# Optimization experiments

Measured on AMD Instinct MI355X. Metric: run time of the kernel, lower is better.

## Reference

```python
import jax, jax.numpy as jnp
import numpy as np

B, S, H, D = 2, 2048, 16, 64
DIM = H * D          # 1024, fused QKV dense outputs 3*DIM
EPS = 1e-6
NINF = -10000.0      # additive mask value from module
STD = 0.02           # truncated-normal init stddev (plain normal here)


def setup_inputs() -> dict:
    key = jax.random.key(0)
    k0, k1, k2 = jax.random.split(key, 3)
    x = jax.random.normal(k0, (B, S, DIM), jnp.float32)
    ln_g = jnp.ones((DIM,), jnp.float32)
    ln_b = jnp.zeros((DIM,), jnp.float32)
    wqkv = jax.random.normal(k1, (DIM, 3 * DIM), jnp.float32) * STD
    bqkv = jnp.zeros((3 * DIM,), jnp.float32)
    wo = jax.random.normal(k2, (DIM, DIM), jnp.float32) * STD
    bo = jnp.zeros((DIM,), jnp.float32)
    return {"x": x, "ln_g": ln_g, "ln_b": ln_b, "wqkv": wqkv,
            "bqkv": bqkv, "wo": wo, "bo": bo}


def reference(x, ln_g, ln_b, wqkv, bqkv, wo, bo):
    b, s, _ = x.shape
    # pre-norm LayerNorm (axis=-1, eps=1e-6)
    mu = jnp.mean(x, axis=-1, keepdims=True)
    var = jnp.mean(jnp.square(x - mu), axis=-1, keepdims=True)
    h = (x - mu) * jax.lax.rsqrt(var + EPS) * ln_g + ln_b
    # fused QKV projection, split along feature axis
    qkv = h @ wqkv + bqkv                       # [b, s, 3*DIM]
    q, k, v = jnp.split(qkv, 3, axis=2)

    def heads(t):                               # [b, s, DIM] -> [b, H, s, D]
        return t.reshape(b, s, H, D).transpose(0, 2, 1, 3)

    q, k, v = heads(q), heads(k), heads(v)
    scores = jnp.einsum("bhqd,bhkd->bhqk", q, k) / jnp.sqrt(jnp.float32(D))
    # causal mask: positions j > i get ninf (mask=None path, Lq == Lk)
    causal = (jnp.arange(s)[:, None] < jnp.arange(s)[None, :]).astype(jnp.float32) * NINF
    a = jax.nn.softmax(scores + causal, axis=-1)  # attdrop rate 0 -> identity
    ctx = jnp.einsum("bhqk,bhkd->bhqd", a, v)
    ctx = ctx.transpose(0, 2, 1, 3).reshape(b, s, DIM)
    # output dense + residual (drop rate 0 -> identity)
    return x + ctx @ wo + bo
```

## Files before the change

kernel.cpp:

```cpp
#include <hip/hip_runtime.h>
#include <hip/hip_bf16.h>

#define B_   2
#define S_   2048
#define H_   16
#define D_   64
#define DIM_ 1024
#define QKV_SZ (32 * 2048 * 64)

typedef __attribute__((ext_vector_type(8))) short bf16x8;
typedef __attribute__((ext_vector_type(4))) float f32x4;
typedef unsigned short u16;
typedef unsigned int u32;

static __device__ __forceinline__ u16 f2bf(float f) {
    union { float f; unsigned u; } v; v.f = f;
    unsigned u = v.u;
    unsigned r = (u + 0x7fffu + ((u >> 16) & 1u)) >> 16;
    return (u16)r;
}
static __device__ __forceinline__ float exp2_fast(float x) {
    float r; asm("v_exp_f32 %0, %1" : "=v"(r) : "v"(x)); return r;
}
static __device__ __forceinline__ u32 cvtpk_bf16(float lo, float hi) {
    u32 r; asm("v_cvt_pk_bf16_f32 %0, %1, %2" : "=v"(r) : "v"(lo), "v"(hi)); return r;
}
static __device__ __forceinline__ void gload_lds16(const u16* g, u16* l) {
    __builtin_amdgcn_global_load_lds(
        (const __attribute__((address_space(1))) void*)g,
        (__attribute__((address_space(3))) void*)l, 16, 0, 0);
}

__global__ __launch_bounds__(256) void prep_kernel(
    const float* __restrict__ x, const float* __restrict__ g,
    const float* __restrict__ b, u16* __restrict__ hb,
    const float* __restrict__ wqkv, u16* __restrict__ wqkvT,
    const float* __restrict__ wo, u16* __restrict__ woT)
{
    __shared__ u16 T[64][65];
    __shared__ float rs[4], rss[4];
    int bid = blockIdx.x;
    int t = threadIdx.x;
    if (bid < 4096) {
        int row = bid;
        const float4 v = ((const float4*)(x + row * DIM_))[t];
        float s  = v.x + v.y + v.z + v.w;
        float ss = v.x*v.x + v.y*v.y + v.z*v.z + v.w*v.w;
#pragma unroll
        for (int m = 1; m < 64; m <<= 1) { s += __shfl_xor(s, m); ss += __shfl_xor(ss, m); }
        int wid = t >> 6, lane = t & 63;
        if (lane == 0) { rs[wid] = s; rss[wid] = ss; }
        __syncthreads();
        s  = rs[0] + rs[1] + rs[2] + rs[3];
        ss = rss[0] + rss[1] + rss[2] + rss[3];
        float mu   = s * (1.0f / DIM_);
        float var  = ss * (1.0f / DIM_) - mu * mu;
        float rstd = rsqrtf(var + 1e-6f);
        const float4 gv = ((const float4*)g)[t];
        const float4 bv = ((const float4*)b)[t];
        ushort4 ov;
        ov.x = f2bf((v.x - mu) * rstd * gv.x + bv.x);
        ov.y = f2bf((v.y - mu) * rstd * gv.y + bv.y);
        ov.z = f2bf((v.z - mu) * rstd * gv.z + bv.z);
        ov.w = f2bf((v.w - mu) * rstd * gv.w + bv.w);
        ((ushort4*)(hb + row * DIM_))[t] = ov;
    } else {
        const float* src; u16* dst; int R, C, c0, r0;
        if (bid < 4864) {
            int idx = bid - 4096;
            src = wqkv; dst = wqkvT; R = 1024; C = 3072;
            c0 = (idx % 48) * 64; r0 = (idx / 48) * 64;
        } else {
            int idx = bid - 4864;
            src = wo; dst = woT; R = 1024; C = 1024;
            c0 = (idx % 16) * 64; r0 = (idx / 16) * 64;
        }
        int rl = t >> 4, cl = (t & 15) * 4;
#pragma unroll
        for (int p = 0; p < 4; p++) {
            float4 v = *(const float4*)(src + (size_t)(r0 + rl + p * 16) * C + c0 + cl);
            T[cl + 0][rl + p * 16] = f2bf(v.x);
            T[cl + 1][rl + p * 16] = f2bf(v.y);
            T[cl + 2][rl + p * 16] = f2bf(v.z);
            T[cl + 3][rl + p * 16] = f2bf(v.w);
        }
        __syncthreads();
#pragma unroll
        for (int p = 0; p < 4; p++) {
            ushort4 o;
            o.x = T[rl + p * 16][cl + 0];
            o.y = T[rl + p * 16][cl + 1];
            o.z = T[rl + p * 16][cl + 2];
            o.w = T[rl + p * 16][cl + 3];
            *(ushort4*)(dst + (size_t)(c0 + rl + p * 16) * R + r0 + cl) = o;
        }
    }
}

__global__ __launch_bounds__(256) void qkv_gemm128(
    const u16* __restrict__ A, const u16* __restrict__ Bw,
    const float* __restrict__ bias, u16* __restrict__ qkv)
{
    __shared__ __align__(16) u16 As[2][128 * 32];
    __shared__ __align__(16) u16 Bs[2][128 * 32];
    int t = threadIdx.x;
    int bn = blockIdx.x * 128, bm = blockIdx.y * 128;
    int wid = t >> 6, lane = t & 63;
    int wm = wid >> 1, wn = wid & 1;
    int l15 = lane & 15, l4 = lane >> 4;

    f32x4 zero = {0.f, 0.f, 0.f, 0.f};
    f32x4 acc[4][4];
#pragma unroll
    for (int i = 0; i < 4; i++)
#pragma unroll
        for (int j = 0; j < 4; j++) acc[i][j] = zero;

    int scol = ((lane & 3) ^ ((lane >> 3) & 3)) * 8;
    const u16* aSrc = A  + (size_t)(bm + wid * 32 + (lane >> 2)) * 1024 + scol;
    const u16* bSrc = Bw + (size_t)(bn + wid * 32 + (lane >> 2)) * 1024 + scol;
    int rdk = ((l15 >> 1) & 3) << 4;

#define STAGE_G(bufsel, kk) do { \
        char* Ad = (char*)As + (bufsel) * 8192 + wid * 2048; \
        char* Bd = (char*)Bs + (bufsel) * 8192 + wid * 2048; \
        gload_lds16(aSrc + (kk),             (u16*)Ad); \
        gload_lds16(aSrc + (kk) + 16 * 1024, (u16*)(Ad + 1024)); \
        gload_lds16(bSrc + (kk),             (u16*)Bd); \
        gload_lds16(bSrc + (kk) + 16 * 1024, (u16*)(Bd + 1024)); \
    } while (0)

    STAGE_G(0, 0);
    __syncthreads();
    int cur = 0;
    for (int kt = 0; kt < 32; ++kt) {
        if (kt < 31) STAGE_G(cur ^ 1, (kt + 1) * 32);
        const char* Ab = (const char*)As + cur * 8192;
        const char* Bb = (const char*)Bs + cur * 8192;
        bf16x8 af[4], bf[4];
#pragma unroll
        for (int mi = 0; mi < 4; mi++)
            af[mi] = *(const bf16x8*)(Ab + (wm * 64 + mi * 16 + l15) * 64 + (l4 * 16 ^ rdk));
#pragma unroll
        for (int ni = 0; ni < 4; ni++)
            bf[ni] = *(const bf16x8*)(Bb + (wn * 64 + ni * 16 + l15) * 64 + (l4 * 16 ^ rdk));
        __builtin_amdgcn_s_setprio(1);
#pragma unroll
        for (int mi = 0; mi < 4; mi++)
#pragma unroll
            for (int ni = 0; ni < 4; ni++)
                acc[mi][ni] = __builtin_amdgcn_mfma_f32_16x16x32_bf16(af[mi], bf[ni], acc[mi][ni], 0, 0, 0);
        __builtin_amdgcn_s_setprio(0);
        __syncthreads();
        cur ^= 1;
    }
#pragma unroll
    for (int mi = 0; mi < 4; mi++)
#pragma unroll
        for (int ni = 0; ni < 4; ni++) {
            int col = bn + wn * 64 + ni * 16 + l15;
            int which = col >> 10, f = col & 1023;
            int hh = f >> 6, d = f & 63;
            float bs = bias[col];
            if (which == 2) {
                int s_base = bm + wm * 64 + mi * 16 + l4 * 4;
                int bb = s_base >> 11, s = s_base & 2047;
                ushort4 pk;
                pk.x = f2bf(acc[mi][ni][0] + bs);
                pk.y = f2bf(acc[mi][ni][1] + bs);
                pk.z = f2bf(acc[mi][ni][2] + bs);
                pk.w = f2bf(acc[mi][ni][3] + bs);
                *(ushort4*)(qkv + (size_t)2 * QKV_SZ +
                            ((size_t)(bb * 16 + hh) * 64 + d) * 2048 + s) = pk;
            } else {
                float scl = (which == 0) ? 0.18033688011112042f : 1.0f;
#pragma unroll
                for (int r = 0; r < 4; r++) {
                    int row = bm + wm * 64 + mi * 16 + l4 * 4 + r;
                    int bb = row >> 11, s = row & 2047;
                    qkv[(size_t)which * QKV_SZ + ((size_t)(bb * 16 + hh) * 2048 + s) * 64 + d] =
                        f2bf((acc[mi][ni][r] + bs) * scl);
                }
            }
        }
}

__global__ __launch_bounds__(256) void out_gemm128(
    const u16* __restrict__ A, const u16* __restrict__ Bw,
    const float* __restrict__ bias, const float* __restrict__ xres,
    float* __restrict__ out)
{
    __shared__ __align__(16) u16 As[2][128 * 32];
    __shared__ __align__(16) u16 Bs[2][64 * 32];
    int t = threadIdx.x;
    int bn = blockIdx.x * 64, bm = blockIdx.y * 128;
    int wid = t >> 6, lane = t & 63;
    int l15 = lane & 15, l4 = lane >> 4;

    f32x4 zero = {0.f, 0.f, 0.f, 0.f};
    f32x4 acc[2][4];
#pragma unroll
    for (int i = 0; i < 2; i++)
#pragma unroll
        for (int j = 0; j < 4; j++) acc[i][j] = zero;

    int scol = ((t & 3) ^ ((t >> 3) & 3)) * 8;
    const u16* aSrc = A  + (size_t)(bm + (t >> 2)) * 1024 + scol;
    const u16* bSrc = Bw + (size_t)(bn + (t >> 2)) * 1024 + scol;
    int rdk = ((l15 >> 1) & 3) << 4;

#define OSTG(bufsel, kk) do { \
        char* Ad = (char*)As + (bufsel) * 8192 + wid * 1024; \
        char* Bd = (char*)Bs + (bufsel) * 4096 + wid * 1024; \
        gload_lds16(aSrc + (kk),             (u16*)Ad); \
        gload_lds16(aSrc + (kk) + 64 * 1024, (u16*)(Ad + 4096)); \
        gload_lds16(bSrc + (kk),             (u16*)Bd); \
    } while (0)

    OSTG(0, 0);
    __syncthreads();
    int cur = 0;
    for (int kt = 0; kt < 32; ++kt) {
        if (kt < 31) OSTG(cur ^ 1, (kt + 1) * 32);
        const char* Ab = (const char*)As + cur * 8192;
        const char* Bb = (const char*)Bs + cur * 4096;
        bf16x8 af[2], bf[4];
#pragma unroll
        for (int mi = 0; mi < 2; mi++)
            af[mi] = *(const bf16x8*)(Ab + (wid * 32 + mi * 16 + l15) * 64 + (l4 * 16 ^ rdk));
#pragma unroll
        for (int ni = 0; ni < 4; ni++)
            bf[ni] = *(const bf16x8*)(Bb + (ni * 16 + l15) * 64 + (l4 * 16 ^ rdk));
        __builtin_amdgcn_s_setprio(1);
#pragma unroll
        for (int mi = 0; mi < 2; mi++)
#pragma unroll
            for (int ni = 0; ni < 4; ni++)
                acc[mi][ni] = __builtin_amdgcn_mfma_f32_16x16x32_bf16(af[mi], bf[ni], acc[mi][ni], 0, 0, 0);
        __builtin_amdgcn_s_setprio(0);
        __syncthreads();
        cur ^= 1;
    }
#pragma unroll
    for (int mi = 0; mi < 2; mi++)
#pragma unroll
        for (int ni = 0; ni < 4; ni++) {
            int col = bn + ni * 16 + l15;
            float bs = bias[col];
#pragma unroll
            for (int r = 0; r < 4; r++) {
                int row = bm + wid * 32 + mi * 16 + l4 * 4 + r;
                out[(size_t)row * 1024 + col] = xres[(size_t)row * 1024 + col] + acc[mi][ni][r] + bs;
            }
        }
}

__global__ __launch_bounds__(256) void attn_kernel(
    const u16* __restrict__ qbuf, const u16* __restrict__ kbuf,
    const u16* __restrict__ vbuf, u16* __restrict__ ctx)
{
    __shared__ __align__(16) char Ks[64 * 128];
    __shared__ __align__(16) char Vt[64 * 128];
    __shared__ __align__(16) char Pb[4 * 16 * 128];

    int t = threadIdx.x, wid = t >> 6, lane = t & 63;
    int l15 = lane & 15, l4 = lane >> 4;
    int idx = blockIdx.x;
    int qt = 31 - (idx >> 5);
    int bh = idx & 31;
    int q0 = qt * 64;
    int sr = t >> 3, g = t & 7;
    int bb = bh >> 4, hh = bh & 15;
    f32x4 zero = {0.f, 0.f, 0.f, 0.f};

    const u16* Q = qbuf + (size_t)(bh * 2048 + q0 + wid * 16) * 64;
    bf16x8 aq0 = *(const bf16x8*)(Q + l15 * 64 + 8 * l4);
    bf16x8 aq1 = *(const bf16x8*)(Q + l15 * 64 + 32 + 8 * l4);

    f32x4 o[4];
#pragma unroll
    for (int f = 0; f < 4; f++) o[f] = zero;
    float m_run = -1e30f;
    float l_run = 0.f;

    int kswz = (16 * g) ^ ((sr & 7) << 4);
    char* Pw = Pb + wid * 2048;
    int prow = l15 * 128;
    int pkey = (l15 & 7) << 4;
    int qloc = wid * 16 + l15;

    const u16* Kbase = kbuf + (size_t)bh * 2048 * 64;
    const u16* Vbase = vbuf + (size_t)bh * 64 * 2048;

    bf16x8 ck0 = *(const bf16x8*)(Kbase + (size_t)sr * 64 + g * 8);
    bf16x8 ck1 = *(const bf16x8*)(Kbase + (size_t)(sr + 32) * 64 + g * 8);
    bf16x8 cv0 = *(const bf16x8*)(Vbase + (size_t)sr * 2048 + g * 8);
    bf16x8 cv1 = *(const bf16x8*)(Vbase + (size_t)(sr + 32) * 2048 + g * 8);

    for (int kt = 0; kt <= qt; ++kt) {
        int nkt = (kt < qt) ? kt + 1 : qt;
        const u16* Kn = Kbase + (size_t)nkt * 64 * 64;
        const u16* Vn = Vbase + (size_t)nkt * 64;
        bf16x8 a = *(const bf16x8*)(Kn + (size_t)sr * 64 + g * 8);
        bf16x8 b = *(const bf16x8*)(Kn + (size_t)(sr + 32) * 64 + g * 8);
        bf16x8 c = *(const bf16x8*)(Vn + (size_t)sr * 2048 + g * 8);
        bf16x8 d = *(const bf16x8*)(Vn + (size_t)(sr + 32) * 2048 + g * 8);
        *(bf16x8*)(Ks + sr * 128 + kswz) = ck0;
        *(bf16x8*)(Ks + (sr + 32) * 128 + kswz) = ck1;
        *(bf16x8*)(Vt + sr * 128 + kswz) = cv0;
        *(bf16x8*)(Vt + (sr + 32) * 128 + kswz) = cv1;
        asm volatile("s_waitcnt lgkmcnt(0)" ::: "memory");
        __builtin_amdgcn_s_barrier();
        asm volatile("" ::: "memory");

        f32x4 sc[4];
        __builtin_amdgcn_s_setprio(1);
#pragma unroll
        for (int nf = 0; nf < 4; ++nf) {
            int krow = nf * 16 + l15;
            int kkey = (krow & 7) << 4;
            bf16x8 kb0 = *(const bf16x8*)(Ks + krow * 128 + ((16 * l4) ^ kkey));
            bf16x8 kb1 = *(const bf16x8*)(Ks + krow * 128 + ((64 + 16 * l4) ^ kkey));
            f32x4 z = zero;
            z = __builtin_amdgcn_mfma_f32_16x16x32_bf16(kb0, aq0, z, 0, 0, 0);
            z = __builtin_amdgcn_mfma_f32_16x16x32_bf16(kb1, aq1, z, 0, 0, 0);
            sc[nf] = z;
        }
        __builtin_amdgcn_s_setprio(0);

        if (kt == qt) {
#pragma unroll
            for (int nf = 0; nf < 4; nf++)
#pragma unroll
                for (int r = 0; r < 4; r++) {
                    int ka = nf * 16 + 4 * l4 + r;
                    if (ka > qloc) sc[nf][r] = -1e30f;
                }
        }
        float lmax = sc[0][0];
#pragma unroll
        for (int nf = 0; nf < 4; nf++)
#pragma unroll
            for (int r = 0; r < 4; r++) lmax = fmaxf(lmax, sc[nf][r]);
        if (__any(lmax > m_run + 10.f)) {
            float m0 = lmax;
            m0 = fmaxf(m0, __shfl_xor(m0, 16));
            m0 = fmaxf(m0, __shfl_xor(m0, 32));
            float mn = fmaxf(m_run, m0);
            float al = exp2_fast(m_run - mn);
            l_run *= al;
            m_run = mn;
            float a0 = __shfl(al, 4 * l4 + 0);
            float a1 = __shfl(al, 4 * l4 + 1);
            float a2 = __shfl(al, 4 * l4 + 2);
            float a3 = __shfl(al, 4 * l4 + 3);
#pragma unroll
            for (int f = 0; f < 4; f++) {
                o[f][0] *= a0; o[f][1] *= a1; o[f][2] *= a2; o[f][3] *= a3;
            }
        }
        float psum = 0.f;
#pragma unroll
        for (int nf = 0; nf < 4; nf++)
#pragma unroll
            for (int r = 0; r < 4; r++) {
                float pv = exp2_fast(sc[nf][r] - m_run);
                sc[nf][r] = pv; psum += pv;
            }
        l_run += psum;
#pragma unroll
        for (int nf = 0; nf < 4; nf++) {
            uint2 w;
            w.x = cvtpk_bf16(sc[nf][0], sc[nf][1]);
            w.y = cvtpk_bf16(sc[nf][2], sc[nf][3]);
            *(uint2*)(Pw + prow + ((nf * 32 + l4 * 8) ^ pkey)) = w;
        }
        __builtin_amdgcn_s_setprio(1);
#pragma unroll
        for (int kk = 0; kk < 2; kk++) {
            bf16x8 pa = *(const bf16x8*)(Pw + prow + ((64 * kk + 16 * l4) ^ pkey));
#pragma unroll
            for (int f = 0; f < 4; f++) {
                int vrow = f * 16 + l15;
                int vkey = (vrow & 7) << 4;
                bf16x8 vb = *(const bf16x8*)(Vt + vrow * 128 + ((64 * kk + 16 * l4) ^ vkey));
                o[f] = __builtin_amdgcn_mfma_f32_16x16x32_bf16(pa, vb, o[f], 0, 0, 0);
            }
        }
        __builtin_amdgcn_s_setprio(0);
        __syncthreads();
        ck0 = a; ck1 = b; cv0 = c; cv1 = d;
    }
    l_run += __shfl_xor(l_run, 16);
    l_run += __shfl_xor(l_run, 32);
#pragma unroll
    for (int r = 0; r < 4; r++) {
        float lr = __shfl(l_run, 4 * l4 + r);
        float inv = 1.f / lr;
        int qa = q0 + wid * 16 + l4 * 4 + r;
        u16* dst = ctx + (size_t)(bb * 2048 + qa) * 1024 + hh * 64;
#pragma unroll
        for (int f = 0; f < 4; f++) dst[f * 16 + l15] = f2bf(o[f][r] * inv);
    }
}

extern "C" void kernel_launch(void* const* d_in, const int* in_sizes, int n_in,
                              void* d_out, int out_size, void* d_ws, size_t ws_size,
                              hipStream_t stream)
{
    const float* x    = (const float*)d_in[0];
    const float* ln_g = (const float*)d_in[1];
    const float* ln_b = (const float*)d_in[2];
    const float* wqkv = (const float*)d_in[3];
    const float* bqkv = (const float*)d_in[4];
    const float* wo   = (const float*)d_in[5];
    const float* bo   = (const float*)d_in[6];
    float* out = (float*)d_out;

    char* ws = (char*)d_ws;
    u16* hbuf  = (u16*)ws;
    u16* qkvb  = (u16*)(ws + 8388608);
    u16* ctxb  = (u16*)(ws + 33554432);
    u16* wqkvT = ctxb;
    u16* woT   = (u16*)(ws + 41943040);

    prep_kernel<<<5120, 256, 0, stream>>>(x, ln_g, ln_b, hbuf, wqkv, wqkvT, wo, woT);
    qkv_gemm128<<<dim3(24, 32), 256, 0, stream>>>(hbuf, wqkvT, bqkv, qkvb);
    attn_kernel<<<1024, 256, 0, stream>>>(
        qkvb, qkvb + QKV_SZ, qkvb + 2 * QKV_SZ, ctxb);
    out_gemm128<<<dim3(16, 32), 256, 0, stream>>>(ctxb, woT, bo, x, out);
}
```

Measured before the change: 115.6 us.

## Enlarge attention query tile to 128 rows, two 16-row blocks per wave

Each attention block now handles 128 query rows instead of 64, and each wave processes two 16-row query sub-blocks. This reuses each K/V tile loaded into shared memory across twice as many queries, halving global K/V traffic and barrier count per query. The causal mask is generalized to per-element checks over the last tiles, and the block order is changed so the first 256 blocks take the longest tiles in descending order while the rest ascend. The grid halves to 512 blocks, which lowers parallelism and raises register pressure from the doubled accumulators.

```diff
diff --git a/kernel.cpp b/kernel.cpp
--- a/kernel.cpp
+++ b/kernel.cpp
@@ -261,33 +261,39 @@
 {
     __shared__ __align__(16) char Ks[64 * 128];
     __shared__ __align__(16) char Vt[64 * 128];
-    __shared__ __align__(16) char Pb[4 * 16 * 128];
+    __shared__ __align__(16) char Pb[4 * 32 * 128];
 
     int t = threadIdx.x, wid = t >> 6, lane = t & 63;
     int l15 = lane & 15, l4 = lane >> 4;
     int idx = blockIdx.x;
-    int qt = 31 - (idx >> 5);
-    int bh = idx & 31;
-    int q0 = qt * 64;
+    int qt, bh;
+    if (idx < 256) { qt = 15 - (idx >> 5); bh = idx & 31; }
+    else           { qt = (idx - 256) >> 5; bh = idx & 31; }
+    int q0 = qt * 128;
+    int ktE = 2 * qt + 1;
     int sr = t >> 3, g = t & 7;
     int bb = bh >> 4, hh = bh & 15;
     f32x4 zero = {0.f, 0.f, 0.f, 0.f};
 
-    const u16* Q = qbuf + (size_t)(bh * 2048 + q0 + wid * 16) * 64;
-    bf16x8 aq0 = *(const bf16x8*)(Q + l15 * 64 + 8 * l4);
-    bf16x8 aq1 = *(const bf16x8*)(Q + l15 * 64 + 32 + 8 * l4);
-
-    f32x4 o[4];
-#pragma unroll
-    for (int f = 0; f < 4; f++) o[f] = zero;
-    float m_run = -1e30f;
-    float l_run = 0.f;
+    const u16* Q = qbuf + (size_t)(bh * 2048 + q0 + wid * 32) * 64;
+    bf16x8 aq[2][2];
+#pragma unroll
+    for (int qb = 0; qb < 2; qb++)
+#pragma unroll
+        for (int h = 0; h < 2; h++)
+            aq[qb][h] = *(const bf16x8*)(Q + (qb * 16 + l15) * 64 + h * 32 + 8 * l4);
+
+    f32x4 o[2][4];
+#pragma unroll
+    for (int qb = 0; qb < 2; qb++)
+#pragma unroll
+        for (int f = 0; f < 4; f++) o[qb][f] = zero;
+    float m_run[2] = {-1e30f, -1e30f};
+    float l_run[2] = {0.f, 0.f};
 
     int kswz = (16 * g) ^ ((sr & 7) << 4);
-    char* Pw = Pb + wid * 2048;
-    int prow = l15 * 128;
+    char* Pw = Pb + wid * 4096;
     int pkey = (l15 & 7) << 4;
-    int qloc = wid * 16 + l15;
 
     const u16* Kbase = kbuf + (size_t)bh * 2048 * 64;
     const u16* Vbase = vbuf + (size_t)bh * 64 * 2048;
@@ -297,8 +303,8 @@
     bf16x8 cv0 = *(const bf16x8*)(Vbase + (size_t)sr * 2048 + g * 8);
     bf16x8 cv1 = *(const bf16x8*)(Vbase + (size_t)(sr + 32) * 2048 + g * 8);
 
-    for (int kt = 0; kt <= qt; ++kt) {
-        int nkt = (kt < qt) ? kt + 1 : qt;
+    for (int kt = 0; kt <= ktE; ++kt) {
+        int nkt = (kt < ktE) ? kt + 1 : ktE;
         const u16* Kn = Kbase + (size_t)nkt * 64 * 64;
         const u16* Vn = Vbase + (size_t)nkt * 64;
         bf16x8 a = *(const bf16x8*)(Kn + (size_t)sr * 64 + g * 8);
@@ -313,7 +319,7 @@
         __builtin_amdgcn_s_barrier();
         asm volatile("" ::: "memory");
 
-        f32x4 sc[4];
+        f32x4 sc[2][4];
         __builtin_amdgcn_s_setprio(1);
 #pragma unroll
         for (int nf = 0; nf < 4; ++nf) {
@@ -321,86 +327,115 @@
             int kkey = (krow & 7) << 4;
             bf16x8 kb0 = *(const bf16x8*)(Ks + krow * 128 + ((16 * l4) ^ kkey));
             bf16x8 kb1 = *(const bf16x8*)(Ks + krow * 128 + ((64 + 16 * l4) ^ kkey));
-            f32x4 z = zero;
-            z = __builtin_amdgcn_mfma_f32_16x16x32_bf16(kb0, aq0, z, 0, 0, 0);
-            z = __builtin_amdgcn_mfma_f32_16x16x32_bf16(kb1, aq1, z, 0, 0, 0);
-            sc[nf] = z;
+#pragma unroll
+            for (int qb = 0; qb < 2; qb++) {
+                f32x4 z = zero;
+                z = __builtin_amdgcn_mfma_f32_16x16x32_bf16(kb0, aq[qb][0], z, 0, 0, 0);
+                z = __builtin_amdgcn_mfma_f32_16x16x32_bf16(kb1, aq[qb][1], z, 0, 0, 0);
+                sc[qb][nf] = z;
+            }
         }
         __builtin_amdgcn_s_setprio(0);
 
-        if (kt == qt) {
+        if (kt * 64 + 63 > q0 + wid * 32) {
+#pragma unroll
+            for (int qb = 0; qb < 2; qb++)
+#pragma unroll
+                for (int nf = 0; nf < 4; nf++)
+#pragma unroll
+                    for (int r = 0; r < 4; r++) {
+                        int ka = kt * 64 + nf * 16 + 4 * l4 + r;
+                        int qg = q0 + wid * 32 + qb * 16 + l15;
+                        if (ka > qg) sc[qb][nf][r] = -1e30f;
+                    }
+        }
+        float lmax[2];
+#pragma unroll
+        for (int qb = 0; qb < 2; qb++) {
+            float lm = sc[qb][0][0];
 #pragma unroll
             for (int nf = 0; nf < 4; nf++)
 #pragma unroll
+                for (int r = 0; r < 4; r++) lm = fmaxf(lm, sc[qb][nf][r]);
+            lmax[qb] = lm;
+        }
+        bool need = (lmax[0] > m_run[0] + 10.f) | (lmax[1] > m_run[1] + 10.f);
+        if (__any(need)) {
+#pragma unroll
+            for (int qb = 0; qb < 2; qb++) {
+                float m0 = lmax[qb];
+                m0 = fmaxf(m0, __shfl_xor(m0, 16));
+                m0 = fmaxf(m0, __shfl_xor(m0, 32));
+                float mn = fmaxf(m_run[qb], m0);
+                float al = exp2_fast(m_run[qb] - mn);
+                l_run[qb] *= al;
+                m_run[qb] = mn;
+                float a0 = __shfl(al, 4 * l4 + 0);
+                float a1 = __shfl(al, 4 * l4 + 1);
+                float a2 = __shfl(al, 4 * l4 + 2);
+                float a3 = __shfl(al, 4 * l4 + 3);
+#pragma unroll
+                for (int f = 0; f < 4; f++) {
+                    o[qb][f][0] *= a0; o[qb][f][1] *= a1;
+                    o[qb][f][2] *= a2; o[qb][f][3] *= a3;
+                }
+            }
+        }
+#pragma unroll
+        for (int qb = 0; qb < 2; qb++) {
+            float psum = 0.f;
+#pragma unroll
+            for (int nf = 0; nf < 4; nf++)
+#pragma unroll
                 for (int r = 0; r < 4; r++) {
-                    int ka = nf * 16 + 4 * l4 + r;
-                    if (ka > qloc) sc[nf][r] = -1e30f;
+                    float pv = exp2_fast(sc[qb][nf][r] - m_run[qb]);
+                    sc[qb][nf][r] = pv; psum += pv;
                 }
-        }
-        float lmax = sc[0][0];
-#pragma unroll
-        for (int nf = 0; nf < 4; nf++)
-#pragma unroll
-            for (int r = 0; r < 4; r++) lmax = fmaxf(lmax, sc[nf][r]);
-        if (__any(lmax > m_run + 10.f)) {
-            float m0 = lmax;
-            m0 = fmaxf(m0, __shfl_xor(m0, 16));
-            m0 = fmaxf(m0, __shfl_xor(m0, 32));
-            float mn = fmaxf(m_run, m0);
-            float al = exp2_fast(m_run - mn);
-            l_run *= al;
-            m_run = mn;
-            float a0 = __shfl(al, 4 * l4 + 0);
-            float a1 = __shfl(al, 4 * l4 + 1);
-            float a2 = __shfl(al, 4 * l4 + 2);
-            float a3 = __shfl(al, 4 * l4 + 3);
-#pragma unroll
-            for (int f = 0; f < 4; f++) {
-                o[f][0] *= a0; o[f][1] *= a1; o[f][2] *= a2; o[f][3] *= a3;
-            }
-        }
-        float psum = 0.f;
-#pragma unroll
-        for (int nf = 0; nf < 4; nf++)
-#pragma unroll
-            for (int r = 0; r < 4; r++) {
-                float pv = exp2_fast(sc[nf][r] - m_run);
-                sc[nf][r] = pv; psum += pv;
-            }
-        l_run += psum;
-#pragma unroll
-        for (int nf = 0; nf < 4; nf++) {
-            uint2 w;
-            w.x = cvtpk_bf16(sc[nf][0], sc[nf][1]);
-            w.y = cvtpk_bf16(sc[nf][2], sc[nf][3]);
-            *(uint2*)(Pw + prow + ((nf * 32 + l4 * 8) ^ pkey)) = w;
+            l_run[qb] += psum;
+            int prow = (qb * 16 + l15) * 128;
+#pragma unroll
+            for (int nf = 0; nf < 4; nf++) {
+                uint2 w;
+                w.x = cvtpk_bf16(sc[qb][nf][0], sc[qb][nf][1]);
+                w.y = cvtpk_bf16(sc[qb][nf][2], sc[qb][nf][3]);
+                *(uint2*)(Pw + prow + ((nf * 32 + l4 * 8) ^ pkey)) = w;
+            }
         }
         __builtin_amdgcn_s_setprio(1);
 #pragma unroll
         for (int kk = 0; kk < 2; kk++) {
-            bf16x8 pa = *(const bf16x8*)(Pw + prow + ((64 * kk + 16 * l4) ^ pkey));
+            bf16x8 pa[2];
+#pragma unroll
+            for (int qb = 0; qb < 2; qb++)
+                pa[qb] = *(const bf16x8*)(Pw + (qb * 16 + l15) * 128 + ((64 * kk + 16 * l4) ^ pkey));
 #pragma unroll
             for (int f = 0; f < 4; f++) {
                 int vrow = f * 16 + l15;
                 int vkey = (vrow & 7) << 4;
                 bf16x8 vb = *(const bf16x8*)(Vt + vrow * 128 + ((64 * kk + 16 * l4) ^ vkey));
-                o[f] = __builtin_amdgcn_mfma_f32_16x16x32_bf16(pa, vb, o[f], 0, 0, 0);
+#pragma unroll
+                for (int qb = 0; qb < 2; qb++)
+                    o[qb][f] = __builtin_amdgcn_mfma_f32_16x16x32_bf16(pa[qb], vb, o[qb][f], 0, 0, 0);
             }
         }
         __builtin_amdgcn_s_setprio(0);
         __syncthreads();
         ck0 = a; ck1 = b; cv0 = c; cv1 = d;
     }
-    l_run += __shfl_xor(l_run, 16);
-    l_run += __shfl_xor(l_run, 32);
-#pragma unroll
-    for (int r = 0; r < 4; r++) {
-        float lr = __shfl(l_run, 4 * l4 + r);
-        float inv = 1.f / lr;
-        int qa = q0 + wid * 16 + l4 * 4 + r;
-        u16* dst = ctx + (size_t)(bb * 2048 + qa) * 1024 + hh * 64;
-#pragma unroll
-        for (int f = 0; f < 4; f++) dst[f * 16 + l15] = f2bf(o[f][r] * inv);
+#pragma unroll
+    for (int qb = 0; qb < 2; qb++) {
+        float lr0 = l_run[qb];
+        lr0 += __shfl_xor(lr0, 16);
+        lr0 += __shfl_xor(lr0, 32);
+#pragma unroll
+        for (int r = 0; r < 4; r++) {
+            float lr = __shfl(lr0, 4 * l4 + r);
+            float inv = 1.f / lr;
+            int qa = q0 + wid * 32 + qb * 16 + l4 * 4 + r;
+            u16* dst = ctx + (size_t)(bb * 2048 + qa) * 1024 + hh * 64;
+#pragma unroll
+            for (int f = 0; f < 4; f++) dst[f * 16 + l15] = f2bf(o[qb][f][r] * inv);
+        }
     }
 }
 
@@ -426,7 +461,7 @@
 
     prep_kernel<<<5120, 256, 0, stream>>>(x, ln_g, ln_b, hbuf, wqkv, wqkvT, wo, woT);
     qkv_gemm128<<<dim3(24, 32), 256, 0, stream>>>(hbuf, wqkvT, bqkv, qkvb);
-    attn_kernel<<<1024, 256, 0, stream>>>(
+    attn_kernel<<<512, 256, 0, stream>>>(
         qkvb, qkvb + QKV_SZ, qkvb + 2 * QKV_SZ, ctxb);
     out_gemm128<<<dim3(16, 32), 256, 0, stream>>>(ctxb, woT, bo, x, out);
 }
```

New measurement: 123.2 us. 1.07x slower.
